# Kernel optimization log

Hardware: AMD Instinct MI355X
Metric: run time of the kernel (lower is better)

## Reference

```python
import jax, jax.numpy as jnp
import numpy as np

B, C, H, W, HEADS, S = 8, 512, 32, 32, 8, 77
CH = C // HEADS  # per-head channels = 64
GROUPS = 32      # GroupNorm32


def setup_inputs() -> dict:
    key = jax.random.key(0)
    ks = jax.random.split(key, 6)
    s = 0.02
    return {
        "x": jax.random.normal(ks[0], (B, C, H, W), jnp.float32),
        "encoder_out": jax.random.normal(ks[1], (B, C, S), jnp.float32),
        "capt_attn_mask": jax.random.bernoulli(ks[2], 0.9, (B, S)),
        "norm_scale": jnp.ones((C,), jnp.float32),
        "norm_bias": jnp.zeros((C,), jnp.float32),
        "qkv_w": jax.random.normal(ks[3], (3 * C, C), jnp.float32) * s,
        "qkv_b": jnp.zeros((3 * C,), jnp.float32),
        "ekv_w": jax.random.normal(ks[4], (2 * C, C), jnp.float32) * s,
        "ekv_b": jnp.zeros((2 * C,), jnp.float32),
        "proj_w": jax.random.normal(ks[5], (C, C), jnp.float32) * s,
        "proj_b": jnp.zeros((C,), jnp.float32),
    }


def reference(x, encoder_out, capt_attn_mask, norm_scale, norm_bias,
              qkv_w, qkv_b, ekv_w, ekv_b, proj_w, proj_b):
    b, c, h, w = x.shape
    T = h * w
    xf = x.reshape(b, c, T)

    # GroupNorm(32) in fp32 (GroupNorm32), affine
    xg = xf.reshape(b, GROUPS, c // GROUPS, T).astype(jnp.float32)
    mu = xg.mean(axis=(2, 3), keepdims=True)
    var = xg.var(axis=(2, 3), keepdims=True)
    nrm = ((xg - mu) * jax.lax.rsqrt(var + 1e-5)).reshape(b, c, T)
    nrm = nrm * norm_scale[None, :, None] + norm_bias[None, :, None]

    # 1x1 conv1d qkv projection: [b, 3c, T]
    qkv = jnp.einsum('oc,bct->bot', qkv_w, nrm) + qkv_b[None, :, None]
    qkv = qkv.reshape(b * HEADS, 3 * CH, T)
    q, k, v = jnp.split(qkv, 3, axis=1)  # each [b*heads, CH, T]

    # encoder kv: [b, 2c, S] -> [b*heads, 2*CH, S]
    ekv = jnp.einsum('oc,bcs->bos', ekv_w, encoder_out) + ekv_b[None, :, None]
    ekv = ekv.reshape(b * HEADS, 2 * CH, S)
    ek, ev = jnp.split(ekv, 2, axis=1)
    k = jnp.concatenate([ek, k], axis=-1)  # [b*heads, CH, S+T]
    v = jnp.concatenate([ev, v], axis=-1)

    scale = 1.0 / np.sqrt(np.sqrt(CH))
    wgt = jnp.einsum('bct,bcs->bts', q * scale, k * scale).astype(jnp.float32)

    # additive mask; torch.tile over dim0 is head-major (row i -> batch i % b),
    # faithfully reproduced; self-attn part (last T cols) is all-visible.
    addm_capt = jnp.where(jnp.tile(capt_attn_mask, (HEADS, 1)), 0.0, -10000.0)
    addm = jnp.concatenate(
        [addm_capt, jnp.zeros((b * HEADS, T), jnp.float32)], axis=1)[:, None, :]
    wgt = jax.nn.softmax(wgt + addm, axis=-1).astype(v.dtype)

    out = jnp.einsum('bts,bcs->bct', wgt, v)  # [b*heads, CH, T]
    out = out.reshape(b, c, T)
    out = jnp.einsum('oc,bct->bot', proj_w, out) + proj_b[None, :, None]
    return (xf + out).reshape(b, c, h, w)
```

## Files before the change

### kernel.cpp

```cpp
#include <hip/hip_runtime.h>
#include <math.h>

#define BB 8
#define TT 1024
#define SS 77

typedef short v8s __attribute__((ext_vector_type(8)));
typedef float v4f __attribute__((ext_vector_type(4)));
typedef unsigned short u16x4 __attribute__((ext_vector_type(4)));
typedef unsigned short u16x8 __attribute__((ext_vector_type(8)));
typedef unsigned short u16;

#define SCALEF 0.424660891f
#define MASKNEG (-14426.95f)

__device__ __forceinline__ u16 f2bf(float f) {
  unsigned u = __float_as_uint(f);
  u = (u + 0x7fffu + ((u >> 16) & 1u)) >> 16;
  return (u16)u;
}
__device__ __forceinline__ u16 hi16(float f) {
  return (u16)(__float_as_uint(f) >> 16);
}
__device__ __forceinline__ float bf2f(u16 u) {
  return __uint_as_float(((unsigned)u) << 16);
}
__device__ __forceinline__ void gl_lds16(const void* g, void* l) {
  __builtin_amdgcn_global_load_lds(
      (const __attribute__((address_space(1))) void*)g,
      (__attribute__((address_space(3))) void*)l, 16, 0, 0);
}

__global__ __launch_bounds__(256) void prep_gn_kernel(
    const float* __restrict__ x, const float* __restrict__ scale,
    const float* __restrict__ bias, u16* __restrict__ nrmT,
    const float* __restrict__ qkv_w, const float* __restrict__ ekv_w,
    const float* __restrict__ proj_w, const float* __restrict__ enc,
    const float* __restrict__ qkv_b, const float* __restrict__ ekv_b,
    u16* __restrict__ wQK, u16* __restrict__ wV, u16* __restrict__ wEK,
    u16* __restrict__ wEV, u16* __restrict__ projwb, u16* __restrict__ encT,
    float* __restrict__ bQK, float* __restrict__ bV,
    float* __restrict__ bEK, float* __restrict__ bEV) {
  __shared__ u16 Xs[16 * 1024];
  __shared__ float red[8];
  int blk = blockIdx.x, tid = threadIdx.x;

  if (blk < 256) {
    int bg = blk;
    int b = bg >> 5, g = bg & 31;
    const float4* x4 = (const float4*)(x + (size_t)bg * 16384);
    float s = 0.f, sq = 0.f;
#pragma unroll
    for (int i = 0; i < 16; ++i) {
      int idx = tid + 256 * i;
      float4 v = x4[idx];
      s += v.x + v.y + v.z + v.w;
      sq += v.x * v.x + v.y * v.y + v.z * v.z + v.w * v.w;
      int c = idx >> 8, t4 = (idx & 255) * 4;
      u16x4 o; o.x = f2bf(v.x); o.y = f2bf(v.y); o.z = f2bf(v.z); o.w = f2bf(v.w);
      *(u16x4*)(Xs + c * 1024 + t4) = o;
    }
#pragma unroll
    for (int off = 32; off > 0; off >>= 1) {
      s += __shfl_down(s, off, 64);
      sq += __shfl_down(sq, off, 64);
    }
    int wave = tid >> 6;
    if ((tid & 63) == 0) { red[wave] = s; red[wave + 4] = sq; }
    __syncthreads();
    float ts = red[0] + red[1] + red[2] + red[3];
    float tq = red[4] + red[5] + red[6] + red[7];
    float mu = ts * (1.0f / 16384.0f);
    float var = tq * (1.0f / 16384.0f) - mu * mu;
    float rs = rsqrtf(var + 1e-5f);
    float scv[16], biv[16];
#pragma unroll
    for (int c = 0; c < 16; ++c) {
      float ss = scale[g * 16 + c] * rs;
      scv[c] = ss;
      biv[c] = bias[g * 16 + c] - mu * ss;
    }
#pragma unroll
    for (int j = 0; j < 4; ++j) {
      int t = tid + 256 * j;
      u16x8 o0, o1;
#pragma unroll
      for (int c = 0; c < 8; ++c)  o0[c] = f2bf(bf2f(Xs[c * 1024 + t]) * scv[c] + biv[c]);
#pragma unroll
      for (int c = 8; c < 16; ++c) o1[c - 8] = f2bf(bf2f(Xs[c * 1024 + t]) * scv[c] + biv[c]);
      u16* dst = nrmT + ((size_t)b * 1024 + t) * 512 + g * 16;
      *(u16x8*)dst = o0;
      *(u16x8*)(dst + 8) = o1;
    }
    return;
  }

  int p = blk - 256;
  if (p < 512) {
    int idx = p * 256 + tid;
    int n = idx >> 7, c4 = (idx & 127) * 4;
    int which = n >> 9, h = (n >> 6) & 7, ch = n & 63;
    int src = h * 192 + which * 64 + ch;
    float4 v = *(const float4*)(qkv_w + (size_t)src * 512 + c4);
    u16x4 o; o.x = f2bf(v.x * SCALEF); o.y = f2bf(v.y * SCALEF);
    o.z = f2bf(v.z * SCALEF); o.w = f2bf(v.w * SCALEF);
    *(u16x4*)(wQK + (size_t)n * 512 + c4) = o;
  } else if (p < 768) {
    int idx = (p - 512) * 256 + tid;
    int n = idx >> 7, c4 = (idx & 127) * 4;
    int h = n >> 6, ch = n & 63;
    int src = h * 192 + 128 + ch;
    float4 v = *(const float4*)(qkv_w + (size_t)src * 512 + c4);
    u16x4 o; o.x = f2bf(v.x); o.y = f2bf(v.y); o.z = f2bf(v.z); o.w = f2bf(v.w);
    *(u16x4*)(wV + (size_t)n * 512 + c4) = o;
  } else if (p < 1024) {
    int idx = (p - 768) * 256 + tid;
    int n = idx >> 7, c4 = (idx & 127) * 4;
    int h = n >> 6, ch = n & 63;
    int src = h * 128 + ch;
    float4 v = *(const float4*)(ekv_w + (size_t)src * 512 + c4);
    u16x4 o; o.x = f2bf(v.x * SCALEF); o.y = f2bf(v.y * SCALEF);
    o.z = f2bf(v.z * SCALEF); o.w = f2bf(v.w * SCALEF);
    *(u16x4*)(wEK + (size_t)n * 512 + c4) = o;
  } else if (p < 1280) {
    int idx = (p - 1024) * 256 + tid;
    int n = idx >> 7, c4 = (idx & 127) * 4;
    int h = n >> 6, ch = n & 63;
    int src = h * 128 + 64 + ch;
    float4 v = *(const float4*)(ekv_w + (size_t)src * 512 + c4);
    u16x4 o; o.x = f2bf(v.x); o.y = f2bf(v.y); o.z = f2bf(v.z); o.w = f2bf(v.w);
    *(u16x4*)(wEV + (size_t)n * 512 + c4) = o;
  } else if (p < 1536) {
    int idx = (p - 1280) * 256 + tid;
    float4 v = ((const float4*)proj_w)[idx];
    u16x4 o; o.x = f2bf(v.x); o.y = f2bf(v.y); o.z = f2bf(v.z); o.w = f2bf(v.w);
    *(u16x4*)(projwb + (size_t)idx * 4) = o;
  } else if (p < 2048) {
    int idx = (p - 1536) * 256 + tid;
    int b = idx >> 14, rem = idx & 16383;
    int s = rem >> 7, c = (rem & 127) * 4;
    u16x4 o; o.x = 0; o.y = 0; o.z = 0; o.w = 0;
    if (s < SS) {
      const float* pp = enc + ((size_t)b * 512 + c) * SS + s;
      o.x = f2bf(pp[0]); o.y = f2bf(pp[SS]); o.z = f2bf(pp[2 * SS]); o.w = f2bf(pp[3 * SS]);
    }
    *(u16x4*)(encT + ((size_t)b * 128 + s) * 512 + c) = o;
  } else {
    for (int i = tid; i < 2560; i += 256) {
      if (i < 1024) {
        int which = i >> 9, h = (i >> 6) & 7, ch = i & 63;
        bQK[i] = qkv_b[h * 192 + which * 64 + ch] * SCALEF;
      } else if (i < 1536) {
        int j = i - 1024; int h = j >> 6, ch = j & 63;
        bV[j] = qkv_b[h * 192 + 128 + ch];
      } else if (i < 2048) {
        int j = i - 1536; int h = j >> 6, ch = j & 63;
        bEK[j] = ekv_b[h * 128 + ch] * SCALEF;
      } else {
        int j = i - 2048; int h = j >> 6, ch = j & 63;
        bEV[j] = ekv_b[h * 128 + 64 + ch];
      }
    }
  }
}

__global__ __launch_bounds__(256) void proj_all(
    const u16* __restrict__ nrmT, const u16* __restrict__ encT,
    const u16* __restrict__ wQK, const u16* __restrict__ wEK,
    const u16* __restrict__ wV, const u16* __restrict__ wEV,
    const float* __restrict__ bQK, const float* __restrict__ bEK,
    const float* __restrict__ bV, const float* __restrict__ bEV,
    u16* __restrict__ Qh, u16* __restrict__ Kfull, u16* __restrict__ Vfull) {
  __shared__ __align__(16) u16 SH[16384];
  u16* As = SH;
  u16* Bs = SH + 8192;

  int job = blockIdx.x, bz = blockIdx.y;
  int tid = threadIdx.x;
  int lane = tid & 63, w = tid >> 6;
  int lan15 = lane & 15, quad = lane >> 4;
  int wm = w >> 1, wn = w & 1;

  int mode, m0, n0;
  const u16 *Ap, *Bp;
  const float* bias;
  u16 *dA = nullptr, *dB = nullptr;
  int TrA = 0, offA = 0, TrB = 0, offB = 0;
  int coff = 0;

  if (job < 64) {
    mode = 3; m0 = (job >> 3) * 128; n0 = (job & 7) * 128;
    Ap = nrmT + (size_t)bz * 1024 * 512; Bp = wQK; bias = bQK;
    dA = Qh; TrA = 1024; offA = 0; dB = Kfull; TrB = 1152; offB = 128;
  } else if (job < 68) {
    mode = 3; m0 = 0; n0 = (job - 64) * 128;
    Ap = encT + (size_t)bz * 128 * 512; Bp = wEK; bias = bEK;
    dA = Kfull; TrA = 1152; offA = 0; dB = Kfull; TrB = 1152; offB = 0;
  } else if (job < 100) {
    int jj = job - 68; mode = 0; m0 = (jj >> 3) * 128; n0 = (jj & 7) * 128;
    Ap = wV; Bp = nrmT + (size_t)bz * 1024 * 512; bias = bV;
    coff = 128;
  } else {
    int jj = job - 100; mode = 0; m0 = jj * 128; n0 = 0;
    Ap = wEV; Bp = encT + (size_t)bz * 128 * 512; bias = bEV;
    coff = 0;
  }

  int srow = lane >> 3;
  int schunk = (lane & 7) ^ srow;
  const char* Ag = (const char*)(Ap + (size_t)(m0 + w * 32 + srow) * 512) + schunk * 16;
  const char* Bg = (const char*)(Bp + (size_t)(n0 + w * 32 + srow) * 512) + schunk * 16;
  char* Al = (char*)As + w * 4096;
  char* Bl = (char*)Bs + w * 4096;

  v4f acc[4][4] = {};

  for (int step = 0; step < 8; ++step) {
    __syncthreads();
    int kb = step * 128;
#pragma unroll
    for (int i = 0; i < 4; ++i) gl_lds16(Ag + kb + i * 8192, Al + i * 1024);
#pragma unroll
    for (int i = 0; i < 4; ++i) gl_lds16(Bg + kb + i * 8192, Bl + i * 1024);
    __syncthreads();

#pragma unroll
    for (int ksub = 0; ksub < 2; ++ksub) {
      int ch = ((ksub * 4 + quad) ^ (lan15 & 7)) * 16;
      v8s a[4], bf[4];
#pragma unroll
      for (int i = 0; i < 4; ++i)
        a[i] = *(const v8s*)((const char*)As + (wm * 64 + i * 16 + lan15) * 128 + ch);
#pragma unroll
      for (int j = 0; j < 4; ++j)
        bf[j] = *(const v8s*)((const char*)Bs + (wn * 64 + j * 16 + lan15) * 128 + ch);
#pragma unroll
      for (int i = 0; i < 4; ++i)
#pragma unroll
        for (int j = 0; j < 4; ++j)
          acc[i][j] = __builtin_amdgcn_mfma_f32_16x16x32_bf16(a[i], bf[j], acc[i][j], 0, 0, 0);
    }
  }

  if (mode == 3) {
    u16* Tr = SH;
    for (int ph = 0; ph < 2; ++ph) {
      __syncthreads();
      if (wn == ph) {
#pragma unroll
        for (int j = 0; j < 4; ++j) {
          int n = n0 + wn * 64 + j * 16 + lan15;
          float bv_ = bias[n];
#pragma unroll
          for (int i = 0; i < 4; ++i)
#pragma unroll
            for (int r = 0; r < 4; ++r)
              Tr[(wm * 64 + i * 16 + quad * 4 + r) * 72 + j * 16 + lan15] =
                  f2bf(acc[i][j][r] + bv_);
        }
      }
      __syncthreads();
      int nb = n0 + ph * 64;
      u16* dst = (nb < 512) ? dA : dB;
      int Trows = (nb < 512) ? TrA : TrB;
      int roff  = (nb < 512) ? offA : offB;
      int hh = (nb & 511) >> 6;
      int row = tid >> 1, seg = (tid & 1) * 32;
      u16* dp = dst + ((size_t)(bz * 8 + hh) * Trows + roff + m0 + row) * 64 + seg;
#pragma unroll
      for (int g = 0; g < 4; ++g)
        *(u16x8*)(dp + g * 8) = *(const u16x8*)(Tr + row * 72 + seg + g * 8);
    }
  } else {
    u16* Tr = SH;
    u16* Cb = Vfull + (size_t)bz * 512 * 1152;
    for (int ph = 0; ph < 2; ++ph) {
      __syncthreads();
      if (wn == ph) {
#pragma unroll
        for (int i = 0; i < 4; ++i) {
          int ob = wm * 64 + i * 16 + quad * 4;
#pragma unroll
          for (int r = 0; r < 4; ++r) {
            float bi = bias[m0 + ob + r];
#pragma unroll
            for (int j = 0; j < 4; ++j)
              Tr[(ob + r) * 72 + j * 16 + lan15] = f2bf(acc[i][j][r] + bi);
          }
        }
      }
      __syncthreads();
      int row = tid >> 1, seg = (tid & 1) * 32;
      u16* dp = Cb + (size_t)(m0 + row) * 1152 + coff + n0 + ph * 64 + seg;
#pragma unroll
      for (int g = 0; g < 4; ++g)
        *(u16x8*)(dp + g * 8) = *(const u16x8*)(Tr + row * 72 + seg + g * 8);
    }
  }
}

__global__ __launch_bounds__(256) void proj_out(
    const u16* __restrict__ A, const u16* __restrict__ B,
    const float* __restrict__ bias, const float* __restrict__ res,
    float* __restrict__ Cf) {
  __shared__ __align__(16) u16 SH[16384];
  u16* As = SH;
  u16* Bs = SH + 8192;

  int tid = threadIdx.x;
  int lane = tid & 63, w = tid >> 6;
  int lan15 = lane & 15, quad = lane >> 4;
  int wm = w >> 1, wn = w & 1;
  int m0 = blockIdx.y * 128, n0 = blockIdx.x * 128;
  int bz = blockIdx.z;
  const u16* Bb = B + (size_t)bz * 1024 * 512;

  int srow = lane >> 3;
  int schunk = (lane & 7) ^ srow;
  const char* Ag = (const char*)(A + (size_t)(m0 + w * 32 + srow) * 512) + schunk * 16;
  const char* Bg = (const char*)(Bb + (size_t)(n0 + w * 32 + srow) * 512) + schunk * 16;
  char* Al = (char*)As + w * 4096;
  char* Bl = (char*)Bs + w * 4096;

  v4f acc[4][4] = {};

  for (int step = 0; step < 8; ++step) {
    __syncthreads();
    int kb = step * 128;
#pragma unroll
    for (int i = 0; i < 4; ++i) gl_lds16(Ag + kb + i * 8192, Al + i * 1024);
#pragma unroll
    for (int i = 0; i < 4; ++i) gl_lds16(Bg + kb + i * 8192, Bl + i * 1024);
    __syncthreads();

#pragma unroll
    for (int ksub = 0; ksub < 2; ++ksub) {
      int ch = ((ksub * 4 + quad) ^ (lan15 & 7)) * 16;
      v8s a[4], bf[4];
#pragma unroll
      for (int i = 0; i < 4; ++i)
        a[i] = *(const v8s*)((const char*)As + (wm * 64 + i * 16 + lan15) * 128 + ch);
#pragma unroll
      for (int j = 0; j < 4; ++j)
        bf[j] = *(const v8s*)((const char*)Bs + (wn * 64 + j * 16 + lan15) * 128 + ch);
#pragma unroll
      for (int i = 0; i < 4; ++i)
#pragma unroll
        for (int j = 0; j < 4; ++j)
          acc[i][j] = __builtin_amdgcn_mfma_f32_16x16x32_bf16(a[i], bf[j], acc[i][j], 0, 0, 0);
    }
  }

  const float* rb = res + (size_t)bz * 512 * 1024;
  float* Cb = Cf + (size_t)bz * 512 * 1024;
#pragma unroll
  for (int i = 0; i < 4; ++i) {
    int ob = m0 + wm * 64 + i * 16 + quad * 4;
#pragma unroll
    for (int r = 0; r < 4; ++r) {
      int o = ob + r;
      float bi = bias[o];
#pragma unroll
      for (int j = 0; j < 4; ++j) {
        int n = n0 + wn * 64 + j * 16 + lan15;
        Cb[(size_t)o * 1024 + n] = acc[i][j][r] + bi + rb[(size_t)o * 1024 + n];
      }
    }
  }
}

#define AOFF_K 0
#define AOFF_V 16384
#define AOFF_P 32768
#define AOFF_AM 51200
#define ASMEM  51712

__global__ __launch_bounds__(256) void attn_kernel(
    const u16* __restrict__ Qh, const u16* __restrict__ Kf,
    const u16* __restrict__ Vf, const int* __restrict__ mask,
    u16* __restrict__ attnT) {
  __shared__ __align__(16) unsigned char smem[ASMEM];
  float* AM = (float*)(smem + AOFF_AM);

  int bh = blockIdx.x, b = bh >> 3, h = bh & 7;
  int t0 = blockIdx.y * 128;
  int tid = threadIdx.x;
  int lane = tid & 63, w = tid >> 6;
  int lan15 = lane & 15, quad = lane >> 4;
  int r8 = lane >> 3, c8 = lane & 7;
  int swE = (c8 ^ r8) * 8;

  const u16* Qb = Qh + (size_t)bh * 1024 * 64;
  const u16* Kb = Kf + (size_t)bh * 1152 * 64;
  const u16* Vb = Vf + (size_t)bh * 64 * 1152;
  char* Pw = (char*)smem + AOFF_P + w * 4608;
  u16* Pu = (u16*)Pw;

  if (tid < 128)
    AM[tid] = (tid < SS) ? ((mask[h * SS + tid] != 0) ? 0.f : MASKNEG) : -1e30f;

#pragma unroll
  for (int i = 0; i < 4; ++i)
    gl_lds16(Qb + (size_t)(t0 + w * 32 + i * 8 + r8) * 64 + swE, Pw + i * 1024);
#pragma unroll
  for (int i = 0; i < 2; ++i) {
    int row = w * 16 + i * 8;
    gl_lds16(Kb + (size_t)(row + r8) * 64 + swE, (char*)smem + AOFF_K + row * 128);
    gl_lds16(Vb + (size_t)(row + r8) * 1152 + swE, (char*)smem + AOFF_V + row * 128);
  }
  __syncthreads();

  v8s aq[2][2];
#pragma unroll
  for (int mt = 0; mt < 2; ++mt)
#pragma unroll
    for (int ks = 0; ks < 2; ++ks)
      aq[mt][ks] = *(const v8s*)(Pw + (mt * 16 + lan15) * 128 +
                                 (((ks * 4 + quad) ^ (lan15 & 7)) * 16));

  v4f O[2][4] = {};
  float lsum[2] = {0.f, 0.f};

  for (int c = 0; c < 18; ++c) {
    int cur = c & 1;
    if (c < 17) {
      int nb = cur ^ 1;
#pragma unroll
      for (int i = 0; i < 2; ++i) {
        int row = w * 16 + i * 8;
        gl_lds16(Kb + (size_t)((c + 1) * 64 + row + r8) * 64 + swE,
                 (char*)smem + AOFF_K + nb * 8192 + row * 128);
        gl_lds16(Vb + (size_t)(row + r8) * 1152 + (c + 1) * 64 + swE,
                 (char*)smem + AOFF_V + nb * 8192 + row * 128);
      }
    }
    const char* Kc = (const char*)smem + AOFF_K + cur * 8192;
    const char* Vc = (const char*)smem + AOFF_V + cur * 8192;

    v4f ST[4][2] = {};
#pragma unroll
    for (int ks = 0; ks < 2; ++ks) {
      int cofs = ((ks * 4 + quad) ^ (lan15 & 7)) * 16;
      v8s bk[4];
#pragma unroll
      for (int nt = 0; nt < 4; ++nt)
        bk[nt] = *(const v8s*)(Kc + (nt * 16 + lan15) * 128 + cofs);
#pragma unroll
      for (int nt = 0; nt < 4; ++nt)
#pragma unroll
        for (int mt = 0; mt < 2; ++mt)
          ST[nt][mt] = __builtin_amdgcn_mfma_f32_16x16x32_bf16(bk[nt], aq[mt][ks], ST[nt][mt], 0, 0, 0);
    }

    if (c < 2) {
#pragma unroll
      for (int nt = 0; nt < 4; ++nt)
#pragma unroll
        for (int r = 0; r < 4; ++r) {
          float a_ = AM[c * 64 + nt * 16 + quad * 4 + r];
#pragma unroll
          for (int mt = 0; mt < 2; ++mt) ST[nt][mt][r] += a_;
        }
    }

#pragma unroll
    for (int mt = 0; mt < 2; ++mt) {
#pragma unroll
      for (int nt = 0; nt < 4; ++nt) {
        float e0 = __builtin_amdgcn_exp2f(ST[nt][mt][0]);
        float e1 = __builtin_amdgcn_exp2f(ST[nt][mt][1]);
        float e2 = __builtin_amdgcn_exp2f(ST[nt][mt][2]);
        float e3 = __builtin_amdgcn_exp2f(ST[nt][mt][3]);
        u16x4 pk; pk.x = hi16(e0); pk.y = hi16(e1); pk.z = hi16(e2); pk.w = hi16(e3);
        *(u16x4*)&Pu[(mt * 16 + lan15) * 72 + nt * 16 + quad * 4] = pk;
        lsum[mt] += (e0 + e1) + (e2 + e3);
      }
    }

#pragma unroll
    for (int ks = 0; ks < 2; ++ks) {
      int cofs = ((ks * 4 + quad) ^ (lan15 & 7)) * 16;
      v8s ap[2], bv[4];
#pragma unroll
      for (int mt = 0; mt < 2; ++mt)
        ap[mt] = *(const v8s*)(Pw + (mt * 16 + lan15) * 144 + ks * 64 + quad * 16);
#pragma unroll
      for (int nc = 0; nc < 4; ++nc)
        bv[nc] = *(const v8s*)(Vc + (nc * 16 + lan15) * 128 + cofs);
#pragma unroll
      for (int mt = 0; mt < 2; ++mt)
#pragma unroll
        for (int nc = 0; nc < 4; ++nc)
          O[mt][nc] = __builtin_amdgcn_mfma_f32_16x16x32_bf16(ap[mt], bv[nc], O[mt][nc], 0, 0, 0);
    }
    __syncthreads();
  }

#pragma unroll
  for (int mt = 0; mt < 2; ++mt) {
    float v = lsum[mt];
    v += __shfl_xor(v, 16, 64);
    v += __shfl_xor(v, 32, 64);
    AM[w * 32 + mt * 16 + lan15] = v;
  }
  __syncthreads();
  float inv[2][4];
#pragma unroll
  for (int mt = 0; mt < 2; ++mt)
#pragma unroll
    for (int r = 0; r < 4; ++r)
      inv[mt][r] = 1.0f / AM[w * 32 + mt * 16 + quad * 4 + r];

  float* Ot = (float*)smem;
#pragma unroll
  for (int mt = 0; mt < 2; ++mt)
#pragma unroll
    for (int nc = 0; nc < 4; ++nc)
#pragma unroll
      for (int r = 0; r < 4; ++r)
        Ot[(w * 32 + mt * 16 + quad * 4 + r) * 68 + nc * 16 + lan15] =
            O[mt][nc][r] * inv[mt][r];
  __syncthreads();
  {
    int row = tid >> 1, seg = (tid & 1) * 32;
    const float* src = Ot + row * 68 + seg;
    u16* dp = attnT + ((size_t)b * 1024 + t0 + row) * 512 + h * 64 + seg;
#pragma unroll
    for (int g = 0; g < 4; ++g) {
      u16x8 o;
#pragma unroll
      for (int k = 0; k < 8; ++k) o[k] = f2bf(src[g * 8 + k]);
      *(u16x8*)(dp + g * 8) = o;
    }
  }
}

extern "C" void kernel_launch(void* const* d_in, const int* in_sizes, int n_in,
                              void* d_out, int out_size, void* d_ws, size_t ws_size,
                              hipStream_t stream) {
  const float* x       = (const float*)d_in[0];
  const float* enc     = (const float*)d_in[1];
  const int*   mask    = (const int*)d_in[2];
  const float* nscale  = (const float*)d_in[3];
  const float* nbias   = (const float*)d_in[4];
  const float* qkv_w   = (const float*)d_in[5];
  const float* qkv_b   = (const float*)d_in[6];
  const float* ekv_w   = (const float*)d_in[7];
  const float* ekv_b   = (const float*)d_in[8];
  const float* proj_w  = (const float*)d_in[9];
  const float* proj_b  = (const float*)d_in[10];
  float* out = (float*)d_out;

  char* ws = (char*)d_ws;
  const size_t MiB = 1048576;
  u16* nrmT   = (u16*)(ws);
  u16* Qh     = (u16*)(ws + 8 * MiB);
  u16* Kfull  = (u16*)(ws + 16 * MiB);
  u16* Vfull  = (u16*)(ws + 26 * MiB);
  u16* attnT  = (u16*)(ws + 36 * MiB);
  u16* encT   = (u16*)(ws + 44 * MiB);
  u16* wQK    = (u16*)(ws + 45 * MiB);
  u16* wV     = (u16*)(ws + 46 * MiB);
  u16* wEK    = (u16*)(ws + 46 * MiB + 524288);
  u16* wEV    = (u16*)(ws + 47 * MiB);
  u16* projwb = (u16*)(ws + 47 * MiB + 524288);
  float* bQK  = (float*)(ws + 48 * MiB);
  float* bV   = (float*)(ws + 48 * MiB + 4096);
  float* bEK  = (float*)(ws + 48 * MiB + 6144);
  float* bEV  = (float*)(ws + 48 * MiB + 8192);

  prep_gn_kernel<<<dim3(2305), dim3(256), 0, stream>>>(
      x, nscale, nbias, nrmT, qkv_w, ekv_w, proj_w, enc, qkv_b, ekv_b,
      wQK, wV, wEK, wEV, projwb, encT, bQK, bV, bEK, bEV);

  proj_all<<<dim3(104, BB), dim3(256), 0, stream>>>(
      nrmT, encT, wQK, wEK, wV, wEV, bQK, bEK, bV, bEV, Qh, Kfull, Vfull);

  attn_kernel<<<dim3(64, 8), dim3(256), 0, stream>>>(
      Qh, Kfull, Vfull, mask, attnT);

  proj_out<<<dim3(8, 4, BB), dim3(256), 0, stream>>>(
      projwb, attnT, proj_b, x, out);
}
```

Measured before the change: 174.8 us.

## Use two waves with 64 query rows each in attention and write output directly

The attention block drops from four waves to two, and each wave now handles 64 query rows instead of 32. Each K/V fragment read from LDS is therefore reused across more MFMAs. The PV MFMA operands are swapped so the output accumulator is transposed, which lets each lane write normalized bf16 output straight to global memory and removes the LDS staging and two block barriers. The cost is more registers per wave and fewer waves per block to hide latency, and launch bounds now request two blocks per CU.

```diff
diff --git a/kernel.cpp b/kernel.cpp
--- a/kernel.cpp
+++ b/kernel.cpp
@@ -375,7 +375,7 @@
 #define AOFF_AM 51200
 #define ASMEM  51712
 
-__global__ __launch_bounds__(256) void attn_kernel(
+__global__ __launch_bounds__(128, 2) void attn_kernel(
     const u16* __restrict__ Qh, const u16* __restrict__ Kf,
     const u16* __restrict__ Vf, const int* __restrict__ mask,
     u16* __restrict__ attnT) {
@@ -393,41 +393,40 @@
   const u16* Qb = Qh + (size_t)bh * 1024 * 64;
   const u16* Kb = Kf + (size_t)bh * 1152 * 64;
   const u16* Vb = Vf + (size_t)bh * 64 * 1152;
-  char* Pw = (char*)smem + AOFF_P + w * 4608;
+  char* Pw = (char*)smem + AOFF_P + w * 9216;
   u16* Pu = (u16*)Pw;
 
-  if (tid < 128)
-    AM[tid] = (tid < SS) ? ((mask[h * SS + tid] != 0) ? 0.f : MASKNEG) : -1e30f;
-
-#pragma unroll
-  for (int i = 0; i < 4; ++i)
-    gl_lds16(Qb + (size_t)(t0 + w * 32 + i * 8 + r8) * 64 + swE, Pw + i * 1024);
-#pragma unroll
-  for (int i = 0; i < 2; ++i) {
-    int row = w * 16 + i * 8;
+  AM[tid] = (tid < SS) ? ((mask[h * SS + tid] != 0) ? 0.f : MASKNEG) : -1e30f;
+
+#pragma unroll
+  for (int i = 0; i < 8; ++i)
+    gl_lds16(Qb + (size_t)(t0 + w * 64 + i * 8 + r8) * 64 + swE, Pw + i * 1024);
+#pragma unroll
+  for (int i = 0; i < 4; ++i) {
+    int row = w * 32 + i * 8;
     gl_lds16(Kb + (size_t)(row + r8) * 64 + swE, (char*)smem + AOFF_K + row * 128);
     gl_lds16(Vb + (size_t)(row + r8) * 1152 + swE, (char*)smem + AOFF_V + row * 128);
   }
   __syncthreads();
 
-  v8s aq[2][2];
-#pragma unroll
-  for (int mt = 0; mt < 2; ++mt)
+  v8s aq[4][2];
+#pragma unroll
+  for (int mt = 0; mt < 4; ++mt)
 #pragma unroll
     for (int ks = 0; ks < 2; ++ks)
       aq[mt][ks] = *(const v8s*)(Pw + (mt * 16 + lan15) * 128 +
                                  (((ks * 4 + quad) ^ (lan15 & 7)) * 16));
 
-  v4f O[2][4] = {};
-  float lsum[2] = {0.f, 0.f};
+  v4f O[4][4] = {};
+  float lsum[4] = {};
 
   for (int c = 0; c < 18; ++c) {
     int cur = c & 1;
     if (c < 17) {
       int nb = cur ^ 1;
 #pragma unroll
-      for (int i = 0; i < 2; ++i) {
-        int row = w * 16 + i * 8;
+      for (int i = 0; i < 4; ++i) {
+        int row = w * 32 + i * 8;
         gl_lds16(Kb + (size_t)((c + 1) * 64 + row + r8) * 64 + swE,
                  (char*)smem + AOFF_K + nb * 8192 + row * 128);
         gl_lds16(Vb + (size_t)(row + r8) * 1152 + (c + 1) * 64 + swE,
@@ -437,7 +436,7 @@
     const char* Kc = (const char*)smem + AOFF_K + cur * 8192;
     const char* Vc = (const char*)smem + AOFF_V + cur * 8192;
 
-    v4f ST[4][2] = {};
+    v4f ST[4][4] = {};
 #pragma unroll
     for (int ks = 0; ks < 2; ++ks) {
       int cofs = ((ks * 4 + quad) ^ (lan15 & 7)) * 16;
@@ -448,7 +447,7 @@
 #pragma unroll
       for (int nt = 0; nt < 4; ++nt)
 #pragma unroll
-        for (int mt = 0; mt < 2; ++mt)
+        for (int mt = 0; mt < 4; ++mt)
           ST[nt][mt] = __builtin_amdgcn_mfma_f32_16x16x32_bf16(bk[nt], aq[mt][ks], ST[nt][mt], 0, 0, 0);
     }
 
@@ -459,12 +458,12 @@
         for (int r = 0; r < 4; ++r) {
           float a_ = AM[c * 64 + nt * 16 + quad * 4 + r];
 #pragma unroll
-          for (int mt = 0; mt < 2; ++mt) ST[nt][mt][r] += a_;
+          for (int mt = 0; mt < 4; ++mt) ST[nt][mt][r] += a_;
         }
     }
 
 #pragma unroll
-    for (int mt = 0; mt < 2; ++mt) {
+    for (int mt = 0; mt < 4; ++mt) {
 #pragma unroll
       for (int nt = 0; nt < 4; ++nt) {
         float e0 = __builtin_amdgcn_exp2f(ST[nt][mt][0]);
@@ -480,57 +479,43 @@
 #pragma unroll
     for (int ks = 0; ks < 2; ++ks) {
       int cofs = ((ks * 4 + quad) ^ (lan15 & 7)) * 16;
-      v8s ap[2], bv[4];
-#pragma unroll
-      for (int mt = 0; mt < 2; ++mt)
+      v8s ap[4], bv[4];
+#pragma unroll
+      for (int mt = 0; mt < 4; ++mt)
         ap[mt] = *(const v8s*)(Pw + (mt * 16 + lan15) * 144 + ks * 64 + quad * 16);
 #pragma unroll
       for (int nc = 0; nc < 4; ++nc)
         bv[nc] = *(const v8s*)(Vc + (nc * 16 + lan15) * 128 + cofs);
 #pragma unroll
-      for (int mt = 0; mt < 2; ++mt)
-#pragma unroll
-        for (int nc = 0; nc < 4; ++nc)
-          O[mt][nc] = __builtin_amdgcn_mfma_f32_16x16x32_bf16(ap[mt], bv[nc], O[mt][nc], 0, 0, 0);
+      for (int nc = 0; nc < 4; ++nc)
+#pragma unroll
+        for (int mt = 0; mt < 4; ++mt)
+          O[nc][mt] = __builtin_amdgcn_mfma_f32_16x16x32_bf16(bv[nc], ap[mt], O[nc][mt], 0, 0, 0);
     }
     __syncthreads();
   }
 
-#pragma unroll
-  for (int mt = 0; mt < 2; ++mt) {
+  float inv[4];
+#pragma unroll
+  for (int mt = 0; mt < 4; ++mt) {
     float v = lsum[mt];
     v += __shfl_xor(v, 16, 64);
     v += __shfl_xor(v, 32, 64);
-    AM[w * 32 + mt * 16 + lan15] = v;
-  }
-  __syncthreads();
-  float inv[2][4];
-#pragma unroll
-  for (int mt = 0; mt < 2; ++mt)
-#pragma unroll
-    for (int r = 0; r < 4; ++r)
-      inv[mt][r] = 1.0f / AM[w * 32 + mt * 16 + quad * 4 + r];
-
-  float* Ot = (float*)smem;
-#pragma unroll
-  for (int mt = 0; mt < 2; ++mt)
-#pragma unroll
-    for (int nc = 0; nc < 4; ++nc)
-#pragma unroll
-      for (int r = 0; r < 4; ++r)
-        Ot[(w * 32 + mt * 16 + quad * 4 + r) * 68 + nc * 16 + lan15] =
-            O[mt][nc][r] * inv[mt][r];
-  __syncthreads();
-  {
-    int row = tid >> 1, seg = (tid & 1) * 32;
-    const float* src = Ot + row * 68 + seg;
-    u16* dp = attnT + ((size_t)b * 1024 + t0 + row) * 512 + h * 64 + seg;
-#pragma unroll
-    for (int g = 0; g < 4; ++g) {
-      u16x8 o;
-#pragma unroll
-      for (int k = 0; k < 8; ++k) o[k] = f2bf(src[g * 8 + k]);
-      *(u16x8*)(dp + g * 8) = o;
+    inv[mt] = 1.0f / v;
+  }
+
+#pragma unroll
+  for (int mt = 0; mt < 4; ++mt) {
+    int t = t0 + w * 64 + mt * 16 + lan15;
+    u16* dp = attnT + ((size_t)b * 1024 + t) * 512 + h * 64 + quad * 4;
+#pragma unroll
+    for (int nc = 0; nc < 4; ++nc) {
+      u16x4 pk;
+      pk.x = f2bf(O[nc][mt][0] * inv[mt]);
+      pk.y = f2bf(O[nc][mt][1] * inv[mt]);
+      pk.z = f2bf(O[nc][mt][2] * inv[mt]);
+      pk.w = f2bf(O[nc][mt][3] * inv[mt]);
+      *(u16x4*)(dp + nc * 16) = pk;
     }
   }
 }
@@ -576,7 +561,7 @@
   proj_all<<<dim3(104, BB), dim3(256), 0, stream>>>(
       nrmT, encT, wQK, wEK, wV, wEV, bQK, bEK, bV, bEV, Qh, Kfull, Vfull);
 
-  attn_kernel<<<dim3(64, 8), dim3(256), 0, stream>>>(
+  attn_kernel<<<dim3(64, 8), dim3(128), 0, stream>>>(
       Qh, Kfull, Vfull, mask, attnT);
 
   proj_out<<<dim3(8, 4, BB), dim3(256), 0, stream>>>(
```

Result: slower. 183.7 us (+5.0%).
